# Optimization experiments

Measured on AMD Instinct MI355X. Metric: run time of the kernel, lower is better.

The kernel has to match this reference:

```python
import jax, jax.numpy as jnp
import numpy as np

H = 768          # hidden_size
NH = 12          # num_attention_heads
DH = H // NH     # attention_head_size = 64
NE_TYPES = 16    # num_edge_types
B, S = 4, 512
N = B * S        # flattened node count
E = 131072       # number of edges


def setup_inputs() -> dict:
    key = jax.random.key(0)
    ks = jax.random.split(key, 12)
    inp = {
        "hidden_states": jax.random.normal(ks[0], (B, S, H), dtype=jnp.float32),
        "Wq": jax.random.normal(ks[1], (H, H), dtype=jnp.float32) * 0.02,
        "bq": jnp.zeros((H,), dtype=jnp.float32),
        "Wk": jax.random.normal(ks[2], (H, H), dtype=jnp.float32) * 0.02,
        "bk": jnp.zeros((H,), dtype=jnp.float32),
        "Wv": jax.random.normal(ks[3], (H, H), dtype=jnp.float32) * 0.02,
        "bv": jnp.zeros((H,), dtype=jnp.float32),
        "rel_key_emb": jax.random.normal(ks[4], (NE_TYPES, DH), dtype=jnp.float32) * 0.02,
        "rel_val_emb": jax.random.normal(ks[5], (NE_TYPES, DH), dtype=jnp.float32) * 0.02,
        "edges_src": jax.random.randint(ks[6], (E,), 0, N, dtype=jnp.int32),
        "edges_tgt": jax.random.randint(ks[7], (E,), 0, N, dtype=jnp.int32),
        "edges_type": jax.random.randint(ks[8], (E,), 0, NE_TYPES, dtype=jnp.int32),
        "edges_pos": jax.random.randint(ks[9], (E,), 0, NE_TYPES, dtype=jnp.int32),
    }
    return inp


def reference(hidden_states, Wq, bq, Wk, bk, Wv, bv, rel_key_emb, rel_val_emb,
              edges_src, edges_tgt, edges_type, edges_pos):
    b, s, h = hidden_states.shape
    n = b * s
    hs = hidden_states.reshape(n, h)
    # Q/K/V projections, split into heads: [N, NH, DH]
    q = (hs @ Wq.T + bq).reshape(n, NH, DH)
    k = (hs @ Wk.T + bk).reshape(n, NH, DH)
    v = (hs @ Wv.T + bv).reshape(n, NH, DH)
    # Edge gather + relative key embedding (broadcast over heads)
    src_key = k[edges_src] + rel_key_emb[edges_pos][:, None, :]      # [E, NH, DH]
    tgt_query = q[edges_tgt]                                          # [E, NH, DH]
    # Unnormalized exp attention scores per edge per head: [E, NH]
    scores = jnp.exp(jnp.sum(tgt_query * src_key, axis=-1) / jnp.sqrt(jnp.float32(DH)))
    # Segment softmax normalization via scatter-add over target nodes
    denom = jax.ops.segment_sum(scores, edges_tgt, num_segments=n)    # [N, NH]
    attn = scores / denom[edges_tgt]                                  # [E, NH]
    # Reweighted per-edge values (the meaningful computed quantity)
    src_val = v[edges_src] + rel_val_emb[edges_pos][:, None, :]       # [E, NH, DH]
    weighted = src_val * attn[:, :, None]                             # [E, NH, DH]
    # NOTE: the original torch forward returns hidden_states unchanged
    # (the attention chain is dead code). We return the computed edge-weighted
    # values as the correctness target for the gather->exp->scatter-softmax chain.
    return weighted
```

## Files before the change

### kernel.cpp

```cpp
#include <hip/hip_runtime.h>
#include <hip/hip_bf16.h>

#define H 768
#define NH 12
#define DH 64
#define NNODES 2048
#define NEDGES 131072

typedef __bf16 bf16x8 __attribute__((ext_vector_type(8)));
typedef float floatx4 __attribute__((ext_vector_type(4)));

#define GLOAD_LDS16(gptr, ldsptr)                                                        \
  __builtin_amdgcn_global_load_lds((const __attribute__((address_space(1))) void*)(gptr), \
                                   (__attribute__((address_space(3))) void*)(ldsptr),     \
                                   16, 0, 0)

__device__ __forceinline__ unsigned short f2bf(float x) {
  union { __hip_bfloat16 h; unsigned short u; } cv;
  cv.h = __float2bfloat16(x);
  return cv.u;
}

__device__ __forceinline__ float bfu2f(unsigned short u) {
  union { float f; unsigned int i; } c;
  c.i = ((unsigned int)u) << 16;
  return c.f;
}

__global__ __launch_bounds__(256)
void convert_kernel(const float* __restrict__ hs,
                    const float* __restrict__ Wq,
                    const float* __restrict__ Wk,
                    const float* __restrict__ Wv,
                    __hip_bfloat16* __restrict__ hsb,
                    __hip_bfloat16* __restrict__ wb,
                    int* __restrict__ hist) {
  int i = blockIdx.x * 256 + threadIdx.x;
  const int n_hs4 = NNODES * H / 4;
  const int n_w4  = H * H / 4;
  if (i < n_hs4) {
    float4 v = ((const float4*)hs)[i];
    ((ushort4*)hsb)[i] = make_ushort4(f2bf(v.x), f2bf(v.y), f2bf(v.z), f2bf(v.w));
    return;
  }
  int j = i - n_hs4;
  if (j < 3 * n_w4) {
    const float* src = (j < n_w4) ? Wq : (j < 2 * n_w4 ? Wk : Wv);
    float4 v = ((const float4*)src)[j % n_w4];
    ((ushort4*)wb)[j] = make_ushort4(f2bf(v.x), f2bf(v.y), f2bf(v.z), f2bf(v.w));
    return;
  }
  int z = j - 3 * n_w4;
  if (z < NNODES / 4) {
    ((int4*)hist)[z] = make_int4(0, 0, 0, 0);
  }
}

__global__ __launch_bounds__(256)
void qkv_gemm(const __hip_bfloat16* __restrict__ A,
              const __hip_bfloat16* __restrict__ Wb,
              const float* __restrict__ b0,
              const float* __restrict__ b1,
              const float* __restrict__ b2,
              float* __restrict__ out,
              __hip_bfloat16* __restrict__ kb) {
  __shared__ __hip_bfloat16 As[64][32];
  __shared__ __hip_bfloat16 Bs[64][32];

  const int t    = threadIdx.x;
  const int wave = t >> 6;
  const int lane = t & 63;
  const int bm   = blockIdx.x * 64;
  const int bn   = blockIdx.y * 64;
  const int mat  = blockIdx.z;

  const __hip_bfloat16* B = Wb + (size_t)mat * H * H;
  const float* bias = (mat == 0) ? b0 : ((mat == 1) ? b1 : b2);

  const int wm = (wave & 1) * 32;
  const int wn = (wave >> 1) * 32;
  const int lr = lane & 15;
  const int lq = lane >> 4;

  floatx4 acc[2][2] = {};

  const int ar = t >> 2;
  const int ac = (t & 3) * 8;
  __hip_bfloat16* AsF = &As[0][0];
  __hip_bfloat16* BsF = &Bs[0][0];

  for (int kt = 0; kt < H; kt += 32) {
    GLOAD_LDS16(A + (size_t)(bm + ar) * H + kt + ac, AsF + t * 8);
    GLOAD_LDS16(B + (size_t)(bn + ar) * H + kt + ac, BsF + t * 8);
    __syncthreads();

    bf16x8 af[2], bfr[2];
#pragma unroll
    for (int i = 0; i < 2; i++)
      af[i] = *(const bf16x8*)&As[wm + i * 16 + lr][lq * 8];
#pragma unroll
    for (int i = 0; i < 2; i++)
      bfr[i] = *(const bf16x8*)&Bs[wn + i * 16 + lr][lq * 8];
#pragma unroll
    for (int mi = 0; mi < 2; mi++)
#pragma unroll
      for (int ni = 0; ni < 2; ni++)
        acc[mi][ni] = __builtin_amdgcn_mfma_f32_16x16x32_bf16(
            af[mi], bfr[ni], acc[mi][ni], 0, 0, 0);
    __syncthreads();
  }

  if (mat == 1) {
#pragma unroll
    for (int ni = 0; ni < 2; ni++) {
      int col = bn + wn + ni * 16 + lr;
      float bv = bias[col];
#pragma unroll
      for (int mi = 0; mi < 2; mi++) {
#pragma unroll
        for (int r = 0; r < 4; r++) {
          int row = bm + wm + mi * 16 + lq * 4 + r;
          kb[(size_t)row * H + col] = __float2bfloat16(acc[mi][ni][r] + bv);
        }
      }
    }
  } else {
    float* C = out + (size_t)mat * NNODES * H;
#pragma unroll
    for (int ni = 0; ni < 2; ni++) {
      int col = bn + wn + ni * 16 + lr;
      float bv = bias[col];
#pragma unroll
      for (int mi = 0; mi < 2; mi++) {
#pragma unroll
        for (int r = 0; r < 4; r++) {
          int row = bm + wm + mi * 16 + lq * 4 + r;
          C[(size_t)row * H + col] = acc[mi][ni][r] + bv;
        }
      }
    }
  }
}

__global__ __launch_bounds__(256)
void hist_kernel(const int* __restrict__ etgt, int* __restrict__ hist) {
  int e = blockIdx.x * 256 + threadIdx.x;
  atomicAdd(&hist[etgt[e]], 1);
}

__global__ __launch_bounds__(256)
void scan_kernel(const int* __restrict__ hist, int* __restrict__ rowptr,
                 int* __restrict__ cursor) {
  __shared__ int part[256];
  int t = threadIdx.x;
  int loc[8];
  int s = 0;
#pragma unroll
  for (int k = 0; k < 8; k++) { loc[k] = s; s += hist[t * 8 + k]; }
  part[t] = s;
  __syncthreads();
  for (int off = 1; off < 256; off <<= 1) {
    int v = (t >= off) ? part[t - off] : 0;
    __syncthreads();
    if (t >= off) part[t] += v;
    __syncthreads();
  }
  int pre = part[t] - s;
#pragma unroll
  for (int k = 0; k < 8; k++) {
    rowptr[t * 8 + k] = pre + loc[k];
    cursor[t * 8 + k] = pre + loc[k];
  }
  if (t == 255) rowptr[NNODES] = part[255];
}

__global__ __launch_bounds__(256)
void scatter_kernel(const int* __restrict__ esrc, const int* __restrict__ etgt,
                    const int* __restrict__ epos,
                    int* __restrict__ cursor,
                    int* __restrict__ src_s, int* __restrict__ pos_s,
                    int* __restrict__ einv) {
  int e = blockIdx.x * 256 + threadIdx.x;
  int tgt = etgt[e];
  int slot = atomicAdd(&cursor[tgt], 1);
  src_s[slot] = esrc[e];
  pos_s[slot] = epos[e];
  einv[e] = slot;
}

__global__ __launch_bounds__(256)
void scores3_kernel(const float* __restrict__ Q,
                    const __hip_bfloat16* __restrict__ Kb,
                    const float* __restrict__ relk,
                    const int* __restrict__ rowptr,
                    const int* __restrict__ src_s, const int* __restrict__ pos_s,
                    float* __restrict__ scores_s, float* __restrict__ denom) {
  const int t    = blockIdx.x;
  const int tid  = threadIdx.x;
  const int wave = tid >> 6;
  const int lane = tid & 63;
  const int g    = lane >> 4;
  const int off  = (lane & 15) * 4;

  __shared__ float Qs[H];
  __shared__ float Rk[16 * DH];
  __shared__ float dpart[4][NH];

  if (tid < 192)
    *(float4*)&Qs[tid * 4] = *(const float4*)(Q + (size_t)t * H + tid * 4);
  *(float4*)&Rk[tid * 4] = *(const float4*)(relk + tid * 4);
  __syncthreads();

  const int beg = rowptr[t], end = rowptr[t + 1];
  float dacc0 = 0.f, dacc1 = 0.f, dacc2 = 0.f;

  for (int i = beg + wave; i < end; i += 4) {
    const int src = src_s[i];
    const int pos = pos_s[i];
    const unsigned short* Kp = (const unsigned short*)(Kb + (size_t)src * H);
    const float4 r4 = *(const float4*)&Rk[pos * DH + off];
    float s[3];
#pragma unroll
    for (int c = 0; c < 3; c++) {
      ushort4 ku = *(const ushort4*)(Kp + c * 256 + lane * 4);
      float4 q4 = *(const float4*)&Qs[c * 256 + lane * 4];
      s[c] = q4.x * (bfu2f(ku.x) + r4.x) + q4.y * (bfu2f(ku.y) + r4.y) +
             q4.z * (bfu2f(ku.z) + r4.z) + q4.w * (bfu2f(ku.w) + r4.w);
    }
#pragma unroll
    for (int m = 1; m < 16; m <<= 1) {
      s[0] += __shfl_xor(s[0], m);
      s[1] += __shfl_xor(s[1], m);
      s[2] += __shfl_xor(s[2], m);
    }
    if ((lane & 15) == 0) {
      float sc0 = __expf(s[0] * 0.125f);
      float sc1 = __expf(s[1] * 0.125f);
      float sc2 = __expf(s[2] * 0.125f);
      scores_s[(size_t)i * NH + g]     = sc0;
      scores_s[(size_t)i * NH + 4 + g] = sc1;
      scores_s[(size_t)i * NH + 8 + g] = sc2;
      dacc0 += sc0; dacc1 += sc1; dacc2 += sc2;
    }
  }

  if ((lane & 15) == 0) {
    dpart[wave][g]     = dacc0;
    dpart[wave][4 + g] = dacc1;
    dpart[wave][8 + g] = dacc2;
  }
  __syncthreads();
  if (tid < NH) {
    denom[(size_t)t * NH + tid] =
        dpart[0][tid] + dpart[1][tid] + dpart[2][tid] + dpart[3][tid];
  }
}

__global__ __launch_bounds__(256)
void weighted_kernel(const float* __restrict__ V, const float* __restrict__ relv,
                     const int* __restrict__ esrc, const int* __restrict__ etgt,
                     const int* __restrict__ epos,
                     const int* __restrict__ einv,
                     const float* __restrict__ scores_s,
                     const float* __restrict__ denom,
                     float* __restrict__ out) {
  const int wave = threadIdx.x >> 6;
  const int lane = threadIdx.x & 63;
  const int e = blockIdx.x * 4 + wave;
  const int src = esrc[e], tgt = etgt[e], pos = epos[e];
  const int sidx = einv[e];
  const int g = lane >> 4;
  const int off = (lane & 15) * 4;

  const float4 r4 = *(const float4*)(relv + pos * DH + off);
#pragma unroll
  for (int c = 0; c < 3; c++) {
    int h = c * 4 + g;
    float a = scores_s[(size_t)sidx * NH + h] / denom[(size_t)tgt * NH + h];
    float4 v4 = *(const float4*)(V + (size_t)src * H + c * 256 + lane * 4);
    floatx4 o;
    o.x = (v4.x + r4.x) * a;
    o.y = (v4.y + r4.y) * a;
    o.z = (v4.z + r4.z) * a;
    o.w = (v4.w + r4.w) * a;
    __builtin_nontemporal_store(o, (floatx4*)(out + (size_t)e * H + c * 256 + lane * 4));
  }
}

extern "C" void kernel_launch(void* const* d_in, const int* in_sizes, int n_in,
                              void* d_out, int out_size, void* d_ws, size_t ws_size,
                              hipStream_t stream) {
  const float* hs   = (const float*)d_in[0];
  const float* Wq   = (const float*)d_in[1];
  const float* bq   = (const float*)d_in[2];
  const float* Wk   = (const float*)d_in[3];
  const float* bk   = (const float*)d_in[4];
  const float* Wv   = (const float*)d_in[5];
  const float* bv   = (const float*)d_in[6];
  const float* relk = (const float*)d_in[7];
  const float* relv = (const float*)d_in[8];
  const int* esrc   = (const int*)d_in[9];
  const int* etgt   = (const int*)d_in[10];
  const int* epos   = (const int*)d_in[12];
  float* out = (float*)d_out;

  char* ws = (char*)d_ws;
  __hip_bfloat16* hsb = (__hip_bfloat16*)ws;
  __hip_bfloat16* wb  = (__hip_bfloat16*)(ws + 3145728);
  float* qkv      = (float*)(ws + 6684672);
  float* scores_s = (float*)(ws + 25559040);
  float* denom    = (float*)(ws + 31850496);
  int* hist       = (int*)(ws + 31948800);
  int* rowptr     = (int*)(ws + 31956992);
  int* cursor     = (int*)(ws + 31965200);
  __hip_bfloat16* kb = (__hip_bfloat16*)(ws + 31973392);
  int* src_s = (int*)ws;
  int* pos_s = (int*)(ws + 524288);
  int* einv  = (int*)(ws + 1048576);

  convert_kernel<<<3266, 256, 0, stream>>>(hs, Wq, Wk, Wv, hsb, wb, hist);

  dim3 grid_gemm(32, 12, 3);
  qkv_gemm<<<grid_gemm, 256, 0, stream>>>(hsb, wb, bq, bk, bv, qkv, kb);

  const float* Qp = qkv;
  const float* Vp = qkv + (size_t)2 * NNODES * H;

  hist_kernel<<<NEDGES / 256, 256, 0, stream>>>(etgt, hist);
  scan_kernel<<<1, 256, 0, stream>>>(hist, rowptr, cursor);
  scatter_kernel<<<NEDGES / 256, 256, 0, stream>>>(esrc, etgt, epos, cursor,
                                                   src_s, pos_s, einv);

  scores3_kernel<<<NNODES, 256, 0, stream>>>(Qp, kb, relk, rowptr, src_s, pos_s,
                                             scores_s, denom);

  weighted_kernel<<<NEDGES / 4, 256, 0, stream>>>(Vp, relv, esrc, etgt, epos,
                                                  einv, scores_s, denom, out);
}
```

Before: 529.8 us.

## Fuse score and weighted-value kernels into one per-target-node edge kernel

Merges the scores kernel and the per-edge weighted-value kernel into a single kernel launched once per target node. The block computes exp scores and the per-head denominator, keeps the reciprocal in LDS, then walks the same CSR edge range again to write the weighted values to each edge's original output row. This removes a kernel launch, the global denom buffer and the separate gathers of src, tgt, pos and einv. In exchange, output writes become scattered by the original edge index, and work per block depends on node degree.

```diff
diff --git a/kernel.cpp b/kernel.cpp
--- a/kernel.cpp
+++ b/kernel.cpp
@@ -179,22 +179,27 @@
                     const int* __restrict__ epos,
                     int* __restrict__ cursor,
                     int* __restrict__ src_s, int* __restrict__ pos_s,
-                    int* __restrict__ einv) {
+                    int* __restrict__ eorig) {
   int e = blockIdx.x * 256 + threadIdx.x;
   int tgt = etgt[e];
   int slot = atomicAdd(&cursor[tgt], 1);
   src_s[slot] = esrc[e];
   pos_s[slot] = epos[e];
-  einv[e] = slot;
-}
-
-__global__ __launch_bounds__(256)
-void scores3_kernel(const float* __restrict__ Q,
-                    const __hip_bfloat16* __restrict__ Kb,
-                    const float* __restrict__ relk,
-                    const int* __restrict__ rowptr,
-                    const int* __restrict__ src_s, const int* __restrict__ pos_s,
-                    float* __restrict__ scores_s, float* __restrict__ denom) {
+  eorig[slot] = e;
+}
+
+__global__ __launch_bounds__(256)
+void edge_fused_kernel(const float* __restrict__ Q,
+                       const __hip_bfloat16* __restrict__ Kb,
+                       const float* __restrict__ V,
+                       const float* __restrict__ relk,
+                       const float* __restrict__ relv,
+                       const int* __restrict__ rowptr,
+                       const int* __restrict__ src_s,
+                       const int* __restrict__ pos_s,
+                       const int* __restrict__ eorig,
+                       float* __restrict__ scores_s,
+                       float* __restrict__ out) {
   const int t    = blockIdx.x;
   const int tid  = threadIdx.x;
   const int wave = tid >> 6;
@@ -203,12 +208,13 @@
   const int off  = (lane & 15) * 4;
 
   __shared__ float Qs[H];
-  __shared__ float Rk[16 * DH];
+  __shared__ float Rs[16 * DH];
   __shared__ float dpart[4][NH];
+  __shared__ float dinv[NH];
 
   if (tid < 192)
     *(float4*)&Qs[tid * 4] = *(const float4*)(Q + (size_t)t * H + tid * 4);
-  *(float4*)&Rk[tid * 4] = *(const float4*)(relk + tid * 4);
+  *(float4*)&Rs[tid * 4] = *(const float4*)(relk + tid * 4);
   __syncthreads();
 
   const int beg = rowptr[t], end = rowptr[t + 1];
@@ -218,7 +224,7 @@
     const int src = src_s[i];
     const int pos = pos_s[i];
     const unsigned short* Kp = (const unsigned short*)(Kb + (size_t)src * H);
-    const float4 r4 = *(const float4*)&Rk[pos * DH + off];
+    const float4 r4 = *(const float4*)&Rs[pos * DH + off];
     float s[3];
 #pragma unroll
     for (int c = 0; c < 3; c++) {
@@ -250,40 +256,32 @@
     dpart[wave][8 + g] = dacc2;
   }
   __syncthreads();
+
+  *(float4*)&Rs[tid * 4] = *(const float4*)(relv + tid * 4);
   if (tid < NH) {
-    denom[(size_t)t * NH + tid] =
-        dpart[0][tid] + dpart[1][tid] + dpart[2][tid] + dpart[3][tid];
-  }
-}
-
-__global__ __launch_bounds__(256)
-void weighted_kernel(const float* __restrict__ V, const float* __restrict__ relv,
-                     const int* __restrict__ esrc, const int* __restrict__ etgt,
-                     const int* __restrict__ epos,
-                     const int* __restrict__ einv,
-                     const float* __restrict__ scores_s,
-                     const float* __restrict__ denom,
-                     float* __restrict__ out) {
-  const int wave = threadIdx.x >> 6;
-  const int lane = threadIdx.x & 63;
-  const int e = blockIdx.x * 4 + wave;
-  const int src = esrc[e], tgt = etgt[e], pos = epos[e];
-  const int sidx = einv[e];
-  const int g = lane >> 4;
-  const int off = (lane & 15) * 4;
-
-  const float4 r4 = *(const float4*)(relv + pos * DH + off);
-#pragma unroll
-  for (int c = 0; c < 3; c++) {
-    int h = c * 4 + g;
-    float a = scores_s[(size_t)sidx * NH + h] / denom[(size_t)tgt * NH + h];
-    float4 v4 = *(const float4*)(V + (size_t)src * H + c * 256 + lane * 4);
-    floatx4 o;
-    o.x = (v4.x + r4.x) * a;
-    o.y = (v4.y + r4.y) * a;
-    o.z = (v4.z + r4.z) * a;
-    o.w = (v4.w + r4.w) * a;
-    __builtin_nontemporal_store(o, (floatx4*)(out + (size_t)e * H + c * 256 + lane * 4));
+    float den = dpart[0][tid] + dpart[1][tid] + dpart[2][tid] + dpart[3][tid];
+    dinv[tid] = 1.0f / den;
+  }
+  __syncthreads();
+
+  for (int i = beg + wave; i < end; i += 4) {
+    const int src = src_s[i];
+    const int pos = pos_s[i];
+    const int e   = eorig[i];
+    const float4 r4 = *(const float4*)&Rs[pos * DH + off];
+#pragma unroll
+    for (int c = 0; c < 3; c++) {
+      int h = c * 4 + g;
+      float a = scores_s[(size_t)i * NH + h] * dinv[h];
+      float4 v4 = *(const float4*)(V + (size_t)src * H + c * 256 + lane * 4);
+      floatx4 o;
+      o.x = (v4.x + r4.x) * a;
+      o.y = (v4.y + r4.y) * a;
+      o.z = (v4.z + r4.z) * a;
+      o.w = (v4.w + r4.w) * a;
+      __builtin_nontemporal_store(
+          o, (floatx4*)(out + (size_t)e * H + c * 256 + lane * 4));
+    }
   }
 }
 
@@ -309,14 +307,13 @@
   __hip_bfloat16* wb  = (__hip_bfloat16*)(ws + 3145728);
   float* qkv      = (float*)(ws + 6684672);
   float* scores_s = (float*)(ws + 25559040);
-  float* denom    = (float*)(ws + 31850496);
   int* hist       = (int*)(ws + 31948800);
   int* rowptr     = (int*)(ws + 31956992);
   int* cursor     = (int*)(ws + 31965200);
   __hip_bfloat16* kb = (__hip_bfloat16*)(ws + 31973392);
   int* src_s = (int*)ws;
   int* pos_s = (int*)(ws + 524288);
-  int* einv  = (int*)(ws + 1048576);
+  int* eorig = (int*)(ws + 1048576);
 
   convert_kernel<<<3266, 256, 0, stream>>>(hs, Wq, Wk, Wv, hsb, wb, hist);
 
@@ -329,11 +326,9 @@
   hist_kernel<<<NEDGES / 256, 256, 0, stream>>>(etgt, hist);
   scan_kernel<<<1, 256, 0, stream>>>(hist, rowptr, cursor);
   scatter_kernel<<<NEDGES / 256, 256, 0, stream>>>(esrc, etgt, epos, cursor,
-                                                   src_s, pos_s, einv);
-
-  scores3_kernel<<<NNODES, 256, 0, stream>>>(Qp, kb, relk, rowptr, src_s, pos_s,
-                                             scores_s, denom);
-
-  weighted_kernel<<<NEDGES / 4, 256, 0, stream>>>(Vp, relv, esrc, etgt, epos,
-                                                  einv, scores_s, denom, out);
-}
+                                                   src_s, pos_s, eorig);
+
+  edge_fused_kernel<<<NNODES, 256, 0, stream>>>(Qp, kb, Vp, relk, relv, rowptr,
+                                                src_s, pos_s, eorig,
+                                                scores_s, out);
+}
```

Result: no change. 526.3 us (-0.7%).
